# Optimization experiments

Measured on AMD Instinct MI355X. Metric: run time of the kernel, lower is better.

The kernel has to match this reference:

```python
import jax, jax.numpy as jnp
import numpy as np

BN_EPS = 1e-5
L2_EPS = 1e-12

def _conv2d(x, w, pad):
    # x: NCHW, w: OIHW
    return jax.lax.conv_general_dilated(
        x, w, window_strides=(1, 1), padding=[(pad, pad), (pad, pad)],
        dimension_numbers=('NCHW', 'OIHW', 'NCHW'))

def _l2norm(x, axis):
    n = jnp.sqrt(jnp.sum(x * x, axis=axis, keepdims=True))
    return x / jnp.maximum(n, L2_EPS)

def setup_inputs() -> dict:
    key = jax.random.key(0)
    ks = jax.random.split(key, 8)
    x = jax.random.normal(ks[0], (16, 512, 32, 32), dtype=jnp.float32)
    w_proj1 = jax.random.normal(ks[1], (512, 512, 3, 3), dtype=jnp.float32) * 0.02
    bn_gamma = jnp.ones((512,), dtype=jnp.float32)
    bn_beta = jnp.zeros((512,), dtype=jnp.float32)
    bn_mean = jnp.zeros((512,), dtype=jnp.float32)
    bn_var = jnp.ones((512,), dtype=jnp.float32)
    w_proj2 = jax.random.normal(ks[2], (512, 512, 3, 3), dtype=jnp.float32) * 0.02
    w_assign = jax.random.normal(ks[3], (64, 512, 1, 1), dtype=jnp.float32)
    centroids = jax.random.uniform(ks[4], (64, 512), dtype=jnp.float32)
    return {'x': x, 'w_proj1': w_proj1, 'bn_gamma': bn_gamma, 'bn_beta': bn_beta,
            'bn_mean': bn_mean, 'bn_var': bn_var, 'w_proj2': w_proj2,
            'w_assign': w_assign, 'centroids': centroids}

def reference(x, w_proj1, bn_gamma, bn_beta, bn_mean, bn_var, w_proj2, w_assign, centroids):
    # projection head: conv3x3 -> BN (eval) -> ReLU -> conv3x3
    h = _conv2d(x, w_proj1, pad=1)
    inv = jax.lax.rsqrt(bn_var + BN_EPS)
    h = (h - bn_mean[None, :, None, None]) * (bn_gamma * inv)[None, :, None, None] + bn_beta[None, :, None, None]
    h = jax.nn.relu(h)
    x_enc = _conv2d(h, w_proj2, pad=1)

    # descriptor-wise L2 normalization over channels
    xn = _l2norm(x_enc, axis=1)
    N, C, H, W = xn.shape
    K = w_assign.shape[0]

    # soft assignment: 1x1 conv -> softmax over clusters
    sa = _conv2d(xn, w_assign, pad=0).reshape(N, K, H * W)  # [N,K,L]
    sa = jax.nn.softmax(sa, axis=1)

    xf = xn.reshape(N, C, H * W)  # [N,C,L]
    # algebraic rewrite of the per-cluster residual loop:
    # vlad[n,k,c] = sum_l sa[n,k,l]*(xf[n,c,l] - cent[k,c])
    vlad = jnp.einsum('nkl,ncl->nkc', sa, xf) - sa.sum(-1)[:, :, None] * centroids[None]
    vlad = _l2norm(vlad, axis=2)          # intra-normalization
    vlad = vlad.reshape(N, K * C)
    vlad = _l2norm(vlad, axis=1)          # global L2 norm
    return (vlad, x_enc)
```

## Files before the change

kernel.cpp:

```cpp
#include <hip/hip_runtime.h>
#include <math.h>


typedef __bf16 bf16x8 __attribute__((ext_vector_type(8)));
typedef float f32x4 __attribute__((ext_vector_type(4)));

#define GLDS16(gp, lp)                                                  \
  __builtin_amdgcn_global_load_lds(                                     \
      (const __attribute__((address_space(1))) void*)(gp),              \
      (__attribute__((address_space(3))) void*)(lp), 16, 0, 0)

template <int MODE>
__global__ __launch_bounds__(256) void conv_gemm(
    const __bf16* __restrict__ in,
    const __bf16* __restrict__ wt,
    const float* __restrict__ scale, const float* __restrict__ shift,
    __bf16* __restrict__ outp) {
  __shared__ __align__(16) __bf16 Hl[6 * 42 * 64];
  __shared__ __align__(16) __bf16 Wl[2 * 128 * 64];

  const int t = threadIdx.x;
  const int bx = blockIdx.x, oT = blockIdx.y;
  const int lane = t & 63, wid = t >> 6;
  const int l16 = lane & 15, q = lane >> 4;
  const int wrow = wid >> 1, wcol = wid & 1;

  const int n = bx >> 3;
  const int trow0 = (bx & 7) * 4;

  const int swr = t >> 3, sp = t & 7;
  const __bf16* wsrc[4];
#pragma unroll
  for (int i = 0; i < 4; ++i)
    wsrc[i] = wt + (size_t)(oT * 128 + 32 * i + swr) * 4608 + sp * 8;

  const __bf16* inb = in + (size_t)n * (1156 * 512);
  const __bf16* hsrc[8];
  bool hval[8];
#pragma unroll
  for (int i = 0; i < 8; ++i) {
    const int jj = t + 256 * i;
    hval[i] = jj < 2016;
    const int hr = jj / 336;
    const int hrem = jj - hr * 336;
    const int hw = hrem >> 3, hc8 = hrem & 7;
    hsrc[i] = inb + ((size_t)((trow0 + hr) * 34 + hw)) * 512 +
              (hc8 ^ (hw & 7)) * 8;
  }

  const int c0 = (q ^ (l16 & 7)) * 8;
  const int c1 = ((4 + q) ^ (l16 & 7)) * 8;
  int aoff[4], prow_[4], pcol_[4];
#pragma unroll
  for (int i = 0; i < 4; ++i) {
    aoff[i] = (wrow * 64 + i * 16 + l16) * 64;
    const int p = wcol * 64 + i * 16 + l16;
    prow_[i] = p >> 5;
    pcol_[i] = p & 31;
  }

  f32x4 acc[4][4];
#pragma unroll
  for (int i = 0; i < 4; ++i)
#pragma unroll
    for (int j = 0; j < 4; ++j) acc[i][j] = (f32x4){0.f, 0.f, 0.f, 0.f};

#pragma unroll
  for (int i = 0; i < 8; ++i)
    if (hval[i]) GLDS16(hsrc[i], Hl + (t + 256 * i) * 8);
#pragma unroll
  for (int i = 0; i < 4; ++i)
    GLDS16(wsrc[i], Wl + (t + 256 * i) * 8);
#pragma unroll
  for (int i = 0; i < 4; ++i)
    GLDS16(wsrc[i] + 512, Wl + 8192 + (t + 256 * i) * 8);
  asm volatile("s_waitcnt vmcnt(4)" ::: "memory");
  __builtin_amdgcn_s_barrier();

  int tap = 0, dh = 0, dw = 0, cc = 0;
  int tap2 = 2, cc2 = 0;

#pragma unroll 1
  for (int s = 0; s < 72; ++s) {
    const int buf = (s & 1) << 13;
    const __bf16* Wb = Wl + buf;

    bf16x8 aw[4][2], bp[4][2];
#pragma unroll
    for (int i = 0; i < 4; ++i) {
      aw[i][0] = *(const bf16x8*)&Wb[aoff[i] + c0];
      aw[i][1] = *(const bf16x8*)&Wb[aoff[i] + c1];
    }
#pragma unroll
    for (int i = 0; i < 4; ++i) {
      const int col = pcol_[i] + dw;
      const int rb = (prow_[i] + dh) * 2688 + col * 64;
      const int xr = col & 7;
      bp[i][0] = *(const bf16x8*)&Hl[rb + (q ^ xr) * 8];
      bp[i][1] = *(const bf16x8*)&Hl[rb + ((4 + q) ^ xr) * 8];
    }
    asm volatile("s_waitcnt lgkmcnt(0)" ::: "memory");
    __builtin_amdgcn_sched_barrier(0);
    __builtin_amdgcn_s_barrier();

    if (tap == 8 && cc < 7) {
#pragma unroll
      for (int i = 0; i < 8; ++i)
        if (hval[i]) GLDS16(hsrc[i] + (cc + 1) * 64, Hl + (t + 256 * i) * 8);
    }
    if (s < 70) {
      const int woffs2 = (tap2 * 8 + cc2) * 64;
#pragma unroll
      for (int i = 0; i < 4; ++i)
        GLDS16(wsrc[i] + woffs2, Wl + buf + (t + 256 * i) * 8);
    }

    __builtin_amdgcn_s_setprio(1);
#pragma unroll
    for (int kh = 0; kh < 2; ++kh)
#pragma unroll
      for (int mt = 0; mt < 4; ++mt)
#pragma unroll
        for (int nt = 0; nt < 4; ++nt)
          acc[mt][nt] = __builtin_amdgcn_mfma_f32_16x16x32_bf16(
              aw[mt][kh], bp[nt][kh], acc[mt][nt], 0, 0, 0);
    __builtin_amdgcn_s_setprio(0);

    if (s < 70)
      asm volatile("s_waitcnt vmcnt(4)" ::: "memory");
    else
      asm volatile("s_waitcnt vmcnt(0)" ::: "memory");
    __builtin_amdgcn_s_barrier();

    ++tap;
    ++dw;
    if (dw == 3) {
      dw = 0;
      ++dh;
    }
    if (tap == 9) {
      tap = 0;
      dh = 0;
      dw = 0;
      ++cc;
    }
    if (++tap2 == 9) {
      tap2 = 0;
      ++cc2;
    }
  }

#pragma unroll
  for (int nt = 0; nt < 4; ++nt) {
    const int m_l = wcol * 64 + nt * 16 + l16;
    const int mg2 = bx * 128 + m_l;
    const int n2 = mg2 >> 10, pix2 = mg2 & 1023;
#pragma unroll
    for (int mt = 0; mt < 4; ++mt) {
      const int ob = oT * 128 + wrow * 64 + mt * 16 + q * 4;
      f32x4 v = acc[mt][nt];
      union {
        __bf16 b[4];
        uint2 u;
      } pk;
      if (MODE == 0) {
        const f32x4 sc = *(const f32x4*)&scale[ob];
        const f32x4 sh = *(const f32x4*)&shift[ob];
#pragma unroll
        for (int r = 0; r < 4; ++r)
          pk.b[r] = (__bf16)fmaxf(v[r] * sc[r] + sh[r], 0.f);
        __bf16* dst = outp +
                      ((size_t)n2 * 1156 + ((pix2 >> 5) + 1) * 34 +
                       ((pix2 & 31) + 1)) * 512 + ob;
        *(uint2*)dst = pk.u;
      } else {
#pragma unroll
        for (int r = 0; r < 4; ++r) pk.b[r] = (__bf16)v[r];
        __bf16* dst = outp + ((size_t)n2 * 1024 + pix2) * 512 + ob;
        *(uint2*)dst = pk.u;
      }
    }
  }
}

__global__ __launch_bounds__(256) void xform(const float* __restrict__ x,
                                             __bf16* __restrict__ xpad) {
  const int n = blockIdx.x >> 5, h = blockIdx.x & 31;
  const int t = threadIdx.x;
  const int w = t & 31, cg = t >> 5;
  const float* src = x + ((size_t)n * 512 + cg * 64) * 1024 + h * 32 + w;
  __bf16* dst =
      xpad + ((size_t)n * 1156 + (h + 1) * 34 + (w + 1)) * 512 + cg * 64;
  union {
    __bf16 b[8];
    uint4 u;
  } pk;
#pragma unroll 1
  for (int jj = 0; jj < 8; ++jj) {
#pragma unroll
    for (int j = 0; j < 8; ++j) pk.b[j] = (__bf16)src[(jj * 8 + j) * 1024];
    *(uint4*)(dst + jj * 8) = pk.u;
  }
}

__global__ __launch_bounds__(256) void expand_x(const __bf16* __restrict__ xebT,
                                                float* __restrict__ xenc,
                                                __bf16* __restrict__ xeb) {
  __shared__ __align__(16) __bf16 Ll[64 * 64];
  const int t = threadIdx.x;
  const int cc = blockIdx.x, ptile = blockIdx.y, n = blockIdx.z;
  const int p0 = ptile * 64, c0 = cc * 64;
#pragma unroll
  for (int i = 0; i < 2; ++i) {
    const int u = t * 2 + i;
    const int pix = u >> 3, c8 = u & 7;
    uint4 v =
        *(const uint4*)&xebT[((size_t)n * 1024 + p0 + pix) * 512 + c0 + c8 * 8];
    *(uint4*)&Ll[pix * 64 + (c8 ^ (pix & 7)) * 8] = v;
  }
  __syncthreads();
  const int c = t >> 2, g = t & 3;
  union {
    float f[4];
    float4 v;
  } fv[4];
  union {
    __bf16 b[16];
    uint4 u[2];
  } bv;
#pragma unroll
  for (int r = 0; r < 16; ++r) {
    const int pix = g * 16 + r;
    __bf16 b = Ll[pix * 64 + ((c >> 3) ^ (pix & 7)) * 8 + (c & 7)];
    bv.b[r] = b;
    fv[r >> 2].f[r & 3] = (float)b;
  }
  float* fd = xenc + ((size_t)n * 512 + c0 + c) * 1024 + p0 + g * 16;
#pragma unroll
  for (int r = 0; r < 4; ++r) *(float4*)(fd + r * 4) = fv[r].v;
  __bf16* bd = xeb + ((size_t)n * 512 + c0 + c) * 1024 + p0 + g * 16;
  *(uint4*)bd = bv.u[0];
  *(uint4*)(bd + 8) = bv.u[1];
}

__global__ __launch_bounds__(256) void assign_softmax(
    const __bf16* __restrict__ xebT, const __bf16* __restrict__ watb,
    __bf16* __restrict__ saPb, float* __restrict__ S) {
  __shared__ __align__(16) __bf16 Al[64 * 32];
  __shared__ __align__(16) __bf16 Wlb[64 * 32];
  __shared__ float Sl[64];
  const int t = threadIdx.x;
  const int pt = blockIdx.x, n = blockIdx.y;
  const int lane = t & 63, wid = t >> 6;
  const int l16 = lane & 15, q = lane >> 4;
  if (t < 64) Sl[t] = 0.f;

  const int arow = t >> 2;
  const __bf16* asrc = xebT + ((size_t)n * 1024 + pt * 64 + arow) * 512 +
                       ((t & 3) ^ ((arow >> 1) & 3)) * 8;
  const __bf16* wsrc = watb + (size_t)(t >> 2) * 512 + (t & 3) * 8;
  const int ldsb = wid * 512;
  const int sw = (q ^ ((l16 >> 1) & 3)) * 8;
  const int pnoff = (t >> 2) * 32 + (t & 3) * 8;

  f32x4 acc[4];
#pragma unroll
  for (int i = 0; i < 4; ++i) acc[i] = (f32x4){0.f, 0.f, 0.f, 0.f};
  float pn = 0.f;

#pragma unroll 1
  for (int kc = 0; kc < 16; ++kc) {
    GLDS16(asrc + kc * 32, Al + ldsb);
    GLDS16(wsrc + kc * 32, Wlb + ldsb);
    __syncthreads();
    {
      bf16x8 v = *(const bf16x8*)&Al[pnoff];
#pragma unroll
      for (int j = 0; j < 8; ++j) {
        float f = (float)v[j];
        pn = fmaf(f, f, pn);
      }
    }
    bf16x8 pf = *(const bf16x8*)&Al[(wid * 16 + l16) * 32 + sw];
    bf16x8 wf[4];
#pragma unroll
    for (int ka = 0; ka < 4; ++ka)
      wf[ka] = *(const bf16x8*)&Wlb[(ka * 16 + l16) * 32 + sw];
#pragma unroll
    for (int ka = 0; ka < 4; ++ka)
      acc[ka] =
          __builtin_amdgcn_mfma_f32_16x16x32_bf16(wf[ka], pf, acc[ka], 0, 0, 0);
    __syncthreads();
  }
  pn += __shfl_xor(pn, 1);
  pn += __shfl_xor(pn, 2);
  const float rn = 1.0f / fmaxf(sqrtf(__shfl(pn, l16 * 4)), 1e-12f);

  float sc[16];
  float m = -3.4e38f;
#pragma unroll
  for (int ka = 0; ka < 4; ++ka)
#pragma unroll
    for (int r = 0; r < 4; ++r) {
      float v = acc[ka][r] * rn;
      sc[ka * 4 + r] = v;
      m = fmaxf(m, v);
    }
  m = fmaxf(m, __shfl_xor(m, 16));
  m = fmaxf(m, __shfl_xor(m, 32));
  float s = 0.f;
#pragma unroll
  for (int j = 0; j < 16; ++j) {
    sc[j] = __expf(sc[j] - m);
    s += sc[j];
  }
  s += __shfl_xor(s, 16);
  s += __shfl_xor(s, 32);
  const float inv = 1.0f / s;
  const int pixg = pt * 64 + wid * 16 + l16;
#pragma unroll
  for (int j = 0; j < 16; ++j) {
    const int k = (j >> 2) * 16 + q * 4 + (j & 3);
    float sa = sc[j] * inv;
    sc[j] = sa;
    saPb[((size_t)n * 64 + k) * 1024 + pixg] = (__bf16)(sa * rn);
  }
#pragma unroll
  for (int j = 0; j < 16; ++j) {
    float v = sc[j];
    v += __shfl_xor(v, 1);
    v += __shfl_xor(v, 2);
    v += __shfl_xor(v, 4);
    v += __shfl_xor(v, 8);
    sc[j] = v;
  }
  if (l16 == 0) {
#pragma unroll
    for (int j = 0; j < 16; ++j)
      atomicAdd(&Sl[(j >> 2) * 16 + q * 4 + (j & 3)], sc[j]);
  }
  __syncthreads();
  if (t < 64) atomicAdd(&S[n * 64 + t], Sl[t]);
}

__global__ __launch_bounds__(256) void vlad_gemm(
    const __bf16* __restrict__ saPb, const __bf16* __restrict__ xeb,
    float* __restrict__ vpart) {
  __shared__ __align__(16) __bf16 Al[64 * 32];
  __shared__ __align__(16) __bf16 Bl[128 * 32];

  const int t = threadIdx.x;
  const int cT = blockIdx.x, n = blockIdx.y, ks = blockIdx.z;
  const int lane = t & 63, wid = t >> 6;
  const int l16 = lane & 15, q = lane >> 4;
  const int wrow = wid >> 1, wcol = wid & 1;

  const int ar = t >> 2, acp = t & 3;
  const __bf16* asrc = saPb + (size_t)n * 65536 + (size_t)ar * 1024 + ks * 256 +
                       (acp ^ ((ar >> 1) & 3)) * 8;
  const int br0 = t >> 2, bcp0 = t & 3;
  const int br1 = (t + 256) >> 2, bcp1 = t & 3;
  const __bf16* bsrc0 = xeb + (size_t)n * 524288 +
                        (size_t)(cT * 128 + br0) * 1024 + ks * 256 +
                        (bcp0 ^ ((br0 >> 1) & 3)) * 8;
  const __bf16* bsrc1 = xeb + (size_t)n * 524288 +
                        (size_t)(cT * 128 + br1) * 1024 + ks * 256 +
                        (bcp1 ^ ((br1 >> 1) & 3)) * 8;

  const int ldsb = wid * 512;
  const int sw = (q ^ ((l16 >> 1) & 3)) * 8;

  f32x4 acc[2][4];
#pragma unroll
  for (int i = 0; i < 2; ++i)
#pragma unroll
    for (int j = 0; j < 4; ++j) acc[i][j] = (f32x4){0.f, 0.f, 0.f, 0.f};

#pragma unroll 1
  for (int kc = 0; kc < 8; ++kc) {
    GLDS16(asrc + kc * 32, Al + ldsb);
    GLDS16(bsrc0 + kc * 32, Bl + ldsb);
    GLDS16(bsrc1 + kc * 32, Bl + 2048 + ldsb);
    __syncthreads();

    bf16x8 af[2], bf[4];
#pragma unroll
    for (int i = 0; i < 2; ++i)
      af[i] = *(const bf16x8*)&Al[(wrow * 32 + i * 16 + l16) * 32 + sw];
#pragma unroll
    for (int i = 0; i < 4; ++i)
      bf[i] = *(const bf16x8*)&Bl[(wcol * 64 + i * 16 + l16) * 32 + sw];
#pragma unroll
    for (int mt = 0; mt < 2; ++mt)
#pragma unroll
      for (int nt = 0; nt < 4; ++nt)
        acc[mt][nt] = __builtin_amdgcn_mfma_f32_16x16x32_bf16(
            af[mt], bf[nt], acc[mt][nt], 0, 0, 0);
    __syncthreads();
  }

  float* vp = vpart + (size_t)(ks * 16 + n) * 32768;
#pragma unroll
  for (int mt = 0; mt < 2; ++mt) {
    const int krow = wrow * 32 + mt * 16 + q * 4;
#pragma unroll
    for (int nt = 0; nt < 4; ++nt) {
      const int ccol = cT * 128 + wcol * 64 + nt * 16 + l16;
#pragma unroll
      for (int r = 0; r < 4; ++r)
        vp[(size_t)(krow + r) * 512 + ccol] = acc[mt][nt][r];
    }
  }
}

__global__ __launch_bounds__(64) void intra_norm(float* __restrict__ vraw,
                                                 const float* __restrict__ vpart,
                                                 const float* __restrict__ S,
                                                 const float* __restrict__ cent,
                                                 float* __restrict__ gss) {
  const int b = blockIdx.x;
  const int n = b >> 6, k = b & 63;
  const int lane = threadIdx.x;
  const float s = S[b];
  float v[8];
  float ss = 0.f;
#pragma unroll
  for (int j = 0; j < 8; ++j) {
    const int c = lane * 8 + j;
    const size_t off = (size_t)b * 512 + c;
    float val = vpart[off] + vpart[524288 + off] + vpart[2 * 524288 + off] +
                vpart[3 * 524288 + off] - s * cent[k * 512 + c];
    v[j] = val;
    ss += val * val;
  }
#pragma unroll
  for (int off = 1; off < 64; off <<= 1) ss += __shfl_xor(ss, off);
  const float rn = 1.0f / fmaxf(sqrtf(ss), 1e-12f);
#pragma unroll
  for (int j = 0; j < 8; ++j) vraw[(size_t)b * 512 + lane * 8 + j] = v[j] * rn;
  if (lane == 0) atomicAdd(&gss[n], ss * rn * rn);
}

__global__ __launch_bounds__(256) void finalize(const float* __restrict__ vraw,
                                                const float* __restrict__ gss,
                                                float* __restrict__ out) {
  const int id = blockIdx.x * 256 + threadIdx.x;
  const int n = id >> 15;
  out[id] = vraw[id] * (1.0f / fmaxf(sqrtf(gss[n]), 1e-12f));
}

__global__ __launch_bounds__(256) void zero_border(__bf16* __restrict__ xpad,
                                                   __bf16* __restrict__ hpad) {
  const int id = blockIdx.x * 256 + threadIdx.x;
  const int n = id / 8448;
  const int rem = id - n * 8448;
  const int pb = rem >> 6;
  const int c8 = rem & 63;
  int h, w;
  if (pb < 34) {
    h = 0;
    w = pb;
  } else if (pb < 68) {
    h = 33;
    w = pb - 34;
  } else {
    const int r2 = pb - 68;
    h = 1 + (r2 >> 1);
    w = (r2 & 1) * 33;
  }
  __bf16* base = blockIdx.y ? hpad : xpad;
  *(uint4*)(base + ((size_t)n * 1156 + h * 34 + w) * 512 + c8 * 8) =
      (uint4){0u, 0u, 0u, 0u};
}

__global__ __launch_bounds__(256) void wt_prep(const float* __restrict__ w1,
                                               const float* __restrict__ w2,
                                               __bf16* __restrict__ wt1,
                                               __bf16* __restrict__ wt2) {
  __shared__ float Lw[4608];
  const int o = blockIdx.x;
  const float* w = blockIdx.y ? w2 : w1;
  __bf16* wt = blockIdx.y ? wt2 : wt1;
  const int t = threadIdx.x;
#pragma unroll
  for (int i = 0; i < 18; ++i)
    Lw[t + 256 * i] = w[(size_t)o * 4608 + t + 256 * i];
  __syncthreads();
#pragma unroll
  for (int i = 0; i < 18; ++i) {
    const int idk = t + 256 * i;
    const int kt = idk >> 6;
    const int p = (idk >> 3) & 7, e = idk & 7;
    const int logical = p ^ (o & 7);
    const int k2 = kt * 64 + logical * 8 + e;
    const int tap = k2 >> 9, ci = k2 & 511;
    wt[(size_t)o * 4608 + idk] = (__bf16)Lw[ci * 9 + tap];
  }
}

__global__ void misc_prep(const float* g, const float* b, const float* m,
                          const float* v, const float* wA, float* scale,
                          float* shift, __bf16* watb, float* Sz) {
  const int i = blockIdx.x * 256 + threadIdx.x;
  if (i < 512) {
    float sc = g[i] / sqrtf(v[i] + 1e-5f);
    scale[i] = sc;
    shift[i] = b[i] - m[i] * sc;
  } else if (i < 512 + 32768) {
    const int id = i - 512;
    const int k = id >> 9, j = id & 511;
    const int kt = j >> 5, cpos = (j >> 3) & 3, e = j & 7;
    const int c = kt * 32 + (cpos ^ ((k >> 1) & 3)) * 8 + e;
    watb[(size_t)k * 512 + j] = (__bf16)wA[(size_t)k * 512 + c];
  } else if (i < 512 + 32768 + 1040) {
    Sz[i - (512 + 32768)] = 0.f;
  }
}

extern "C" void kernel_launch(void* const* d_in, const int* in_sizes, int n_in,
                              void* d_out, int out_size, void* d_ws,
                              size_t ws_size, hipStream_t stream) {
  const float* x = (const float*)d_in[0];
  const float* w1 = (const float*)d_in[1];
  const float* gam = (const float*)d_in[2];
  const float* bet = (const float*)d_in[3];
  const float* mean = (const float*)d_in[4];
  const float* var = (const float*)d_in[5];
  const float* w2 = (const float*)d_in[6];
  const float* wA = (const float*)d_in[7];
  const float* cent = (const float*)d_in[8];
  float* out = (float*)d_out;

  char* ws = (char*)d_ws;
  __bf16* Wt1 = (__bf16*)(ws + 0);
  __bf16* Wt2 = (__bf16*)(ws + 4718592);
  __bf16* xpad = (__bf16*)(ws + 9437184);
  __bf16* xebT = (__bf16*)(ws + 9437184);
  __bf16* saPb = (__bf16*)(ws + 26214400);
  __bf16* hpad = (__bf16*)(ws + 28377088);
  __bf16* xeb = (__bf16*)(ws + 28377088);
  float* vpart = (float*)(ws + 0);
  float* vraw = (float*)(ws + 8388608);
  float* scale = (float*)(ws + 47316992);
  float* shift = (float*)(ws + 47319040);
  __bf16* watb = (__bf16*)(ws + 47321088);
  float* S = (float*)(ws + 47386624);
  float* gss = (float*)(ws + 47390720);

  float* xenc = out + 524288;

  zero_border<<<dim3(528, 2), 256, 0, stream>>>(xpad, hpad);
  misc_prep<<<135, 256, 0, stream>>>(gam, bet, mean, var, wA, scale, shift,
                                     watb, S);
  wt_prep<<<dim3(512, 2), 256, 0, stream>>>(w1, w2, Wt1, Wt2);
  xform<<<512, 256, 0, stream>>>(x, xpad);

  conv_gemm<0><<<dim3(128, 4), 256, 0, stream>>>(xpad, Wt1, scale, shift, hpad);
  conv_gemm<1><<<dim3(128, 4), 256, 0, stream>>>(hpad, Wt2, nullptr, nullptr,
                                                 xebT);

  expand_x<<<dim3(8, 16, 16), 256, 0, stream>>>(xebT, xenc, xeb);
  assign_softmax<<<dim3(16, 16), 256, 0, stream>>>(xebT, watb, saPb, S);
  vlad_gemm<<<dim3(4, 16, 4), 256, 0, stream>>>(saPb, xeb, vpart);
  intra_norm<<<1024, 64, 0, stream>>>(vraw, vpart, S, cent, gss);
  finalize<<<2048, 256, 0, stream>>>(vraw, gss, out);
}
```

Measured before the change: 316.0 us.

## Merge prep kernels into one launch and multi-buffer assign/vlad GEMM loads

Combines the four preprocessing kernels (border zeroing, BN/assign-weight prep, input transpose, weight repack) into a single launch selected by block index, which removes launch gaps. The input transpose now issues all 64 loads up front instead of looping eight at a time. The assign_softmax and vlad_gemm kernels move from single-buffered LDS with two __syncthreads per step to a 4-stage ring that prefetches three steps ahead, using explicit vmcnt waits and raw barriers. This overlaps global loads with MFMA work, at the cost of more LDS and hand-written wait counts that must match exactly.

```diff
diff --git a/kernel.cpp b/kernel.cpp
--- a/kernel.cpp
+++ b/kernel.cpp
@@ -183,26 +183,6 @@
   }
 }
 
-__global__ __launch_bounds__(256) void xform(const float* __restrict__ x,
-                                             __bf16* __restrict__ xpad) {
-  const int n = blockIdx.x >> 5, h = blockIdx.x & 31;
-  const int t = threadIdx.x;
-  const int w = t & 31, cg = t >> 5;
-  const float* src = x + ((size_t)n * 512 + cg * 64) * 1024 + h * 32 + w;
-  __bf16* dst =
-      xpad + ((size_t)n * 1156 + (h + 1) * 34 + (w + 1)) * 512 + cg * 64;
-  union {
-    __bf16 b[8];
-    uint4 u;
-  } pk;
-#pragma unroll 1
-  for (int jj = 0; jj < 8; ++jj) {
-#pragma unroll
-    for (int j = 0; j < 8; ++j) pk.b[j] = (__bf16)src[(jj * 8 + j) * 1024];
-    *(uint4*)(dst + jj * 8) = pk.u;
-  }
-}
-
 __global__ __launch_bounds__(256) void expand_x(const __bf16* __restrict__ xebT,
                                                 float* __restrict__ xenc,
                                                 __bf16* __restrict__ xeb) {
@@ -246,8 +226,8 @@
 __global__ __launch_bounds__(256) void assign_softmax(
     const __bf16* __restrict__ xebT, const __bf16* __restrict__ watb,
     __bf16* __restrict__ saPb, float* __restrict__ S) {
-  __shared__ __align__(16) __bf16 Al[64 * 32];
-  __shared__ __align__(16) __bf16 Wlb[64 * 32];
+  __shared__ __align__(16) __bf16 Al[4][64 * 32];
+  __shared__ __align__(16) __bf16 Wlb[4][64 * 32];
   __shared__ float Sl[64];
   const int t = threadIdx.x;
   const int pt = blockIdx.x, n = blockIdx.y;
@@ -268,29 +248,45 @@
   for (int i = 0; i < 4; ++i) acc[i] = (f32x4){0.f, 0.f, 0.f, 0.f};
   float pn = 0.f;
 
+#pragma unroll
+  for (int p = 0; p < 3; ++p) {
+    GLDS16(asrc + p * 32, (__bf16*)Al[p] + ldsb);
+    GLDS16(wsrc + p * 32, (__bf16*)Wlb[p] + ldsb);
+  }
+  asm volatile("s_waitcnt vmcnt(4)" ::: "memory");
+  __builtin_amdgcn_s_barrier();
+
 #pragma unroll 1
   for (int kc = 0; kc < 16; ++kc) {
-    GLDS16(asrc + kc * 32, Al + ldsb);
-    GLDS16(wsrc + kc * 32, Wlb + ldsb);
-    __syncthreads();
-    {
-      bf16x8 v = *(const bf16x8*)&Al[pnoff];
-#pragma unroll
-      for (int j = 0; j < 8; ++j) {
-        float f = (float)v[j];
-        pn = fmaf(f, f, pn);
-      }
-    }
-    bf16x8 pf = *(const bf16x8*)&Al[(wid * 16 + l16) * 32 + sw];
+    const __bf16* Ab = Al[kc & 3];
+    const __bf16* Wb = Wlb[kc & 3];
+    bf16x8 pv = *(const bf16x8*)&Ab[pnoff];
+    bf16x8 pf = *(const bf16x8*)&Ab[(wid * 16 + l16) * 32 + sw];
     bf16x8 wf[4];
 #pragma unroll
     for (int ka = 0; ka < 4; ++ka)
-      wf[ka] = *(const bf16x8*)&Wlb[(ka * 16 + l16) * 32 + sw];
+      wf[ka] = *(const bf16x8*)&Wb[(ka * 16 + l16) * 32 + sw];
+    asm volatile("s_waitcnt lgkmcnt(0)" ::: "memory");
+    __builtin_amdgcn_sched_barrier(0);
+    __builtin_amdgcn_s_barrier();
+    if (kc + 3 < 16) {
+      GLDS16(asrc + (kc + 3) * 32, (__bf16*)Al[(kc + 3) & 3] + ldsb);
+      GLDS16(wsrc + (kc + 3) * 32, (__bf16*)Wlb[(kc + 3) & 3] + ldsb);
+    }
+#pragma unroll
+    for (int j = 0; j < 8; ++j) {
+      float f = (float)pv[j];
+      pn = fmaf(f, f, pn);
+    }
 #pragma unroll
     for (int ka = 0; ka < 4; ++ka)
       acc[ka] =
           __builtin_amdgcn_mfma_f32_16x16x32_bf16(wf[ka], pf, acc[ka], 0, 0, 0);
-    __syncthreads();
+    if (kc < 13)
+      asm volatile("s_waitcnt vmcnt(4)" ::: "memory");
+    else
+      asm volatile("s_waitcnt vmcnt(0)" ::: "memory");
+    __builtin_amdgcn_s_barrier();
   }
   pn += __shfl_xor(pn, 1);
   pn += __shfl_xor(pn, 2);
@@ -346,8 +342,8 @@
 __global__ __launch_bounds__(256) void vlad_gemm(
     const __bf16* __restrict__ saPb, const __bf16* __restrict__ xeb,
     float* __restrict__ vpart) {
-  __shared__ __align__(16) __bf16 Al[64 * 32];
-  __shared__ __align__(16) __bf16 Bl[128 * 32];
+  __shared__ __align__(16) __bf16 Al[4][64 * 32];
+  __shared__ __align__(16) __bf16 Bl[4][128 * 32];
 
   const int t = threadIdx.x;
   const int cT = blockIdx.x, n = blockIdx.y, ks = blockIdx.z;
@@ -376,27 +372,45 @@
 #pragma unroll
     for (int j = 0; j < 4; ++j) acc[i][j] = (f32x4){0.f, 0.f, 0.f, 0.f};
 
+#pragma unroll
+  for (int p = 0; p < 3; ++p) {
+    GLDS16(asrc + p * 32, (__bf16*)Al[p] + ldsb);
+    GLDS16(bsrc0 + p * 32, (__bf16*)Bl[p] + ldsb);
+    GLDS16(bsrc1 + p * 32, (__bf16*)Bl[p] + 2048 + ldsb);
+  }
+  asm volatile("s_waitcnt vmcnt(6)" ::: "memory");
+  __builtin_amdgcn_s_barrier();
+
 #pragma unroll 1
   for (int kc = 0; kc < 8; ++kc) {
-    GLDS16(asrc + kc * 32, Al + ldsb);
-    GLDS16(bsrc0 + kc * 32, Bl + ldsb);
-    GLDS16(bsrc1 + kc * 32, Bl + 2048 + ldsb);
-    __syncthreads();
-
+    const __bf16* Ab = Al[kc & 3];
+    const __bf16* Bb = Bl[kc & 3];
     bf16x8 af[2], bf[4];
 #pragma unroll
     for (int i = 0; i < 2; ++i)
-      af[i] = *(const bf16x8*)&Al[(wrow * 32 + i * 16 + l16) * 32 + sw];
+      af[i] = *(const bf16x8*)&Ab[(wrow * 32 + i * 16 + l16) * 32 + sw];
 #pragma unroll
     for (int i = 0; i < 4; ++i)
-      bf[i] = *(const bf16x8*)&Bl[(wcol * 64 + i * 16 + l16) * 32 + sw];
+      bf[i] = *(const bf16x8*)&Bb[(wcol * 64 + i * 16 + l16) * 32 + sw];
+    asm volatile("s_waitcnt lgkmcnt(0)" ::: "memory");
+    __builtin_amdgcn_sched_barrier(0);
+    __builtin_amdgcn_s_barrier();
+    if (kc + 3 < 8) {
+      GLDS16(asrc + (kc + 3) * 32, (__bf16*)Al[(kc + 3) & 3] + ldsb);
+      GLDS16(bsrc0 + (kc + 3) * 32, (__bf16*)Bl[(kc + 3) & 3] + ldsb);
+      GLDS16(bsrc1 + (kc + 3) * 32, (__bf16*)Bl[(kc + 3) & 3] + 2048 + ldsb);
+    }
 #pragma unroll
     for (int mt = 0; mt < 2; ++mt)
 #pragma unroll
       for (int nt = 0; nt < 4; ++nt)
         acc[mt][nt] = __builtin_amdgcn_mfma_f32_16x16x32_bf16(
             af[mt], bf[nt], acc[mt][nt], 0, 0, 0);
-    __syncthreads();
+    if (kc < 5)
+      asm volatile("s_waitcnt vmcnt(6)" ::: "memory");
+    else
+      asm volatile("s_waitcnt vmcnt(0)" ::: "memory");
+    __builtin_amdgcn_s_barrier();
   }
 
   float* vp = vpart + (size_t)(ks * 16 + n) * 32768;
@@ -449,71 +463,95 @@
   out[id] = vraw[id] * (1.0f / fmaxf(sqrtf(gss[n]), 1e-12f));
 }
 
-__global__ __launch_bounds__(256) void zero_border(__bf16* __restrict__ xpad,
-                                                   __bf16* __restrict__ hpad) {
-  const int id = blockIdx.x * 256 + threadIdx.x;
-  const int n = id / 8448;
-  const int rem = id - n * 8448;
-  const int pb = rem >> 6;
-  const int c8 = rem & 63;
-  int h, w;
-  if (pb < 34) {
-    h = 0;
-    w = pb;
-  } else if (pb < 68) {
-    h = 33;
-    w = pb - 34;
+__global__ __launch_bounds__(256) void prep_all(
+    const float* __restrict__ x, const float* __restrict__ w1,
+    const float* __restrict__ w2, const float* __restrict__ g,
+    const float* __restrict__ b, const float* __restrict__ m,
+    const float* __restrict__ v, const float* __restrict__ wA,
+    __bf16* __restrict__ xpad, __bf16* __restrict__ hpad,
+    __bf16* __restrict__ wt1, __bf16* __restrict__ wt2,
+    float* __restrict__ scale, float* __restrict__ shift,
+    __bf16* __restrict__ watb, float* __restrict__ Sz) {
+  __shared__ float Lw[4608];
+  const int bx = blockIdx.x;
+  const int t = threadIdx.x;
+
+  if (bx < 1056) {
+    const int which = bx >= 528;
+    const int id = (which ? bx - 528 : bx) * 256 + t;
+    const int n = id / 8448;
+    const int rem = id - n * 8448;
+    const int pb = rem >> 6;
+    const int c8 = rem & 63;
+    int h, w;
+    if (pb < 34) {
+      h = 0;
+      w = pb;
+    } else if (pb < 68) {
+      h = 33;
+      w = pb - 34;
+    } else {
+      const int r2 = pb - 68;
+      h = 1 + (r2 >> 1);
+      w = (r2 & 1) * 33;
+    }
+    __bf16* base = which ? hpad : xpad;
+    *(uint4*)(base + ((size_t)n * 1156 + h * 34 + w) * 512 + c8 * 8) =
+        (uint4){0u, 0u, 0u, 0u};
+  } else if (bx < 1191) {
+    const int i = (bx - 1056) * 256 + t;
+    if (i < 512) {
+      float sc = g[i] / sqrtf(v[i] + 1e-5f);
+      scale[i] = sc;
+      shift[i] = b[i] - m[i] * sc;
+    } else if (i < 512 + 32768) {
+      const int id = i - 512;
+      const int k = id >> 9, j = id & 511;
+      const int kt = j >> 5, cpos = (j >> 3) & 3, e = j & 7;
+      const int c = kt * 32 + (cpos ^ ((k >> 1) & 3)) * 8 + e;
+      watb[(size_t)k * 512 + j] = (__bf16)wA[(size_t)k * 512 + c];
+    } else if (i < 512 + 32768 + 1040) {
+      Sz[i - (512 + 32768)] = 0.f;
+    }
+  } else if (bx < 1703) {
+    const int bb = bx - 1191;
+    const int n = bb >> 5, h = bb & 31;
+    const int w = t & 31, cg = t >> 5;
+    const float* src = x + ((size_t)n * 512 + cg * 64) * 1024 + h * 32 + w;
+    __bf16* dst =
+        xpad + ((size_t)n * 1156 + (h + 1) * 34 + (w + 1)) * 512 + cg * 64;
+    float fv[64];
+#pragma unroll
+    for (int j = 0; j < 64; ++j) fv[j] = src[j * 1024];
+#pragma unroll
+    for (int jj = 0; jj < 8; ++jj) {
+      union {
+        __bf16 b8[8];
+        uint4 u;
+      } pk;
+#pragma unroll
+      for (int j = 0; j < 8; ++j) pk.b8[j] = (__bf16)fv[jj * 8 + j];
+      *(uint4*)(dst + jj * 8) = pk.u;
+    }
   } else {
-    const int r2 = pb - 68;
-    h = 1 + (r2 >> 1);
-    w = (r2 & 1) * 33;
-  }
-  __bf16* base = blockIdx.y ? hpad : xpad;
-  *(uint4*)(base + ((size_t)n * 1156 + h * 34 + w) * 512 + c8 * 8) =
-      (uint4){0u, 0u, 0u, 0u};
-}
-
-__global__ __launch_bounds__(256) void wt_prep(const float* __restrict__ w1,
-                                               const float* __restrict__ w2,
-                                               __bf16* __restrict__ wt1,
-                                               __bf16* __restrict__ wt2) {
-  __shared__ float Lw[4608];
-  const int o = blockIdx.x;
-  const float* w = blockIdx.y ? w2 : w1;
-  __bf16* wt = blockIdx.y ? wt2 : wt1;
-  const int t = threadIdx.x;
-#pragma unroll
-  for (int i = 0; i < 18; ++i)
-    Lw[t + 256 * i] = w[(size_t)o * 4608 + t + 256 * i];
-  __syncthreads();
-#pragma unroll
-  for (int i = 0; i < 18; ++i) {
-    const int idk = t + 256 * i;
-    const int kt = idk >> 6;
-    const int p = (idk >> 3) & 7, e = idk & 7;
-    const int logical = p ^ (o & 7);
-    const int k2 = kt * 64 + logical * 8 + e;
-    const int tap = k2 >> 9, ci = k2 & 511;
-    wt[(size_t)o * 4608 + idk] = (__bf16)Lw[ci * 9 + tap];
-  }
-}
-
-__global__ void misc_prep(const float* g, const float* b, const float* m,
-                          const float* v, const float* wA, float* scale,
-                          float* shift, __bf16* watb, float* Sz) {
-  const int i = blockIdx.x * 256 + threadIdx.x;
-  if (i < 512) {
-    float sc = g[i] / sqrtf(v[i] + 1e-5f);
-    scale[i] = sc;
-    shift[i] = b[i] - m[i] * sc;
-  } else if (i < 512 + 32768) {
-    const int id = i - 512;
-    const int k = id >> 9, j = id & 511;
-    const int kt = j >> 5, cpos = (j >> 3) & 3, e = j & 7;
-    const int c = kt * 32 + (cpos ^ ((k >> 1) & 3)) * 8 + e;
-    watb[(size_t)k * 512 + j] = (__bf16)wA[(size_t)k * 512 + c];
-  } else if (i < 512 + 32768 + 1040) {
-    Sz[i - (512 + 32768)] = 0.f;
+    const int bb = bx - 1703;
+    const int o = bb & 511;
+    const float* w = (bb >> 9) ? w2 : w1;
+    __bf16* wt = (bb >> 9) ? wt2 : wt1;
+#pragma unroll
+    for (int i = 0; i < 18; ++i)
+      Lw[t + 256 * i] = w[(size_t)o * 4608 + t + 256 * i];
+    __syncthreads();
+#pragma unroll
+    for (int i = 0; i < 18; ++i) {
+      const int idk = t + 256 * i;
+      const int kt = idk >> 6;
+      const int p = (idk >> 3) & 7, e = idk & 7;
+      const int logical = p ^ (o & 7);
+      const int k2 = kt * 64 + logical * 8 + e;
+      const int tap = k2 >> 9, ci = k2 & 511;
+      wt[(size_t)o * 4608 + idk] = (__bf16)Lw[ci * 9 + tap];
+    }
   }
 }
 
@@ -549,11 +587,8 @@
 
   float* xenc = out + 524288;
 
-  zero_border<<<dim3(528, 2), 256, 0, stream>>>(xpad, hpad);
-  misc_prep<<<135, 256, 0, stream>>>(gam, bet, mean, var, wA, scale, shift,
-                                     watb, S);
-  wt_prep<<<dim3(512, 2), 256, 0, stream>>>(w1, w2, Wt1, Wt2);
-  xform<<<512, 256, 0, stream>>>(x, xpad);
+  prep_all<<<2727, 256, 0, stream>>>(x, w1, w2, gam, bet, mean, var, wA, xpad,
+                                     hpad, Wt1, Wt2, scale, shift, watb, S);
 
   conv_gemm<0><<<dim3(128, 4), 256, 0, stream>>>(xpad, Wt1, scale, shift, hpad);
   conv_gemm<1><<<dim3(128, 4), 256, 0, stream>>>(hpad, Wt2, nullptr, nullptr,
```

After: 309.6 us. 2.0% less time.
